# Performance work log

Hardware: AMD Instinct MI355X
Metric: run time of the kernel (lower is better)

Reference implementation:

```python
import jax, jax.numpy as jnp
import numpy as np

N = 8192      # num nodes
E = 131072    # num edges (avg degree 16)
B = 2         # batch
F_NODE = 128
F_EDGE = 64
H = 256       # hidden_dim
L = 3         # num_layers


def setup_inputs() -> dict:
    key = jax.random.key(0)
    ks = jax.random.split(key, 16)
    # unique edges, sorted row-major to match the original i-then-j loop order
    rng = np.random.default_rng(0)
    lin = np.sort(rng.choice(N * N, size=E, replace=False))
    src = jnp.asarray(lin // N, dtype=jnp.int32)
    dst = jnp.asarray(lin % N, dtype=jnp.int32)
    adjacency = jnp.zeros((N, N), jnp.float32).at[src, dst].set(1.0)

    s = 0.05
    return {
        "node_features": jax.random.normal(ks[0], (B, N, F_NODE), jnp.float32),
        "edge_features": jax.random.normal(ks[1], (B, E, F_EDGE), jnp.float32),
        "adjacency": adjacency,
        "src_idx": src,
        "dst_idx": dst,
        "W_ne": jax.random.normal(ks[2], (F_NODE, H), jnp.float32) * s,
        "b_ne": jnp.zeros((H,), jnp.float32),
        "W_ee": jax.random.normal(ks[3], (F_EDGE, H), jnp.float32) * s,
        "b_ee": jnp.zeros((H,), jnp.float32),
        "W_conv": jax.random.normal(ks[4], (L, H, H), jnp.float32) * s,
        "b_conv": jnp.zeros((L, H), jnp.float32),
        "W_cls": jax.random.normal(ks[5], (H, 5), jnp.float32) * s,
        "b_cls": jnp.zeros((5,), jnp.float32),
        "W_ep": jax.random.normal(ks[6], (2 * H, 1), jnp.float32) * s,
        "b_ep": jnp.zeros((1,), jnp.float32),
        "W_gp": jax.random.normal(ks[7], (H, 1), jnp.float32) * s,
        "b_gp": jnp.zeros((1,), jnp.float32),
    }


def reference(node_features, edge_features, adjacency, src_idx, dst_idx,
              W_ne, b_ne, W_ee, b_ee, W_conv, b_conv,
              W_cls, b_cls, W_ep, b_ep, W_gp, b_gp):
    # embeddings (eval mode: dropout is identity)
    h = jax.nn.relu(node_features @ W_ne + b_ne)          # [B,N,H]
    e = jax.nn.relu(edge_features @ W_ee + b_ee)          # [B,E,H] (computed, unused downstream as in original)
    # message-passing layers: messages = A @ h, then linear+relu+residual
    for l in range(L):
        m = jnp.einsum('ij,bjh->bih', adjacency, h)       # dense adjacency matmul
        o = jax.nn.relu(m @ W_conv[l] + b_conv[l])
        h = o + h                                          # residual (in==out dim)
    node_health = h @ W_cls + b_cls                        # [B,N,5]
    # fused edge prediction over all nonzero adjacency entries (row-major order)
    h_src = h[:, src_idx, :]                               # [B,E,H]
    h_dst = h[:, dst_idx, :]                               # [B,E,H]
    edge_repr = jnp.concatenate([h_src, h_dst], axis=-1)   # [B,E,2H]
    edge_propagation = jax.nn.sigmoid(edge_repr @ W_ep + b_ep)  # [B,E,1]
    global_repr = jnp.mean(h, axis=1)                      # [B,H]
    system_health = jax.nn.sigmoid(global_repr @ W_gp + b_gp)   # [B,1]
    return (node_health, edge_propagation, system_health, h)
```

## Files before the change

kernel.cpp:

```cpp
#include <hip/hip_runtime.h>
#include <hip/hip_bf16.h>

typedef __bf16 bf16_t;
typedef __bf16 bf16x8 __attribute__((ext_vector_type(8)));
typedef float f32x4 __attribute__((ext_vector_type(4)));

#define N_NODES 8192
#define N_EDGES 131072
#define HDIM    256


__device__ inline int rowblk_swz(int x) {
  int xcd = x & 7, q = x >> 3;
  return (xcd >> 2) * 128 + (xcd & 3) * 32 + q;
}

__device__ inline float wred(float v) {
#pragma unroll
  for (int m = 32; m; m >>= 1) v += __shfl_xor(v, m);
  return v;
}

__global__ __launch_bounds__(256) void prep_k(const int* __restrict__ src, int* __restrict__ rp,
                                              const float* __restrict__ Wne,
                                              const float* __restrict__ Wconv,
                                              bf16_t* __restrict__ WneT,
                                              bf16_t* __restrict__ WconvT) {
  int x = blockIdx.x, tid = threadIdx.x;
  if (x < 33) {
    int i = x * 256 + tid;
    if (i < N_NODES) {
      int lo = 0, hi = N_EDGES;
      while (lo < hi) { int mid = (lo + hi) >> 1; if (src[mid] < i) lo = mid + 1; else hi = mid; }
      rp[i] = lo;
    } else if (i == N_NODES) {
      rp[i] = N_EDGES;
    }
  } else {
    int t = (x - 33) * 256 + tid;
    if (t < 32768) {
      int n = t / 128, k = t % 128;
      WneT[t] = (bf16_t)Wne[k * 256 + n];
    } else {
      int u = t - 32768;
      int l = u / 65536, r = u % 65536;
      int n = r / 256, k = r % 256;
      WconvT[l * 65536 + n * 256 + k] = (bf16_t)Wconv[l * 65536 + k * 256 + n];
    }
  }
}

__global__ __launch_bounds__(256) void gemm1_k(const float* __restrict__ A,
                                               const bf16_t* __restrict__ BT,
                                               const float* __restrict__ bias,
                                               float* __restrict__ Hout,
                                               bf16_t* __restrict__ S16) {
  int tid = threadIdx.x;
  int lane = tid & 63, wv = tid >> 6;
  int r0 = (rowblk_swz(blockIdx.x) * 4 + wv) * 16;
  int cg0 = blockIdx.y * 64;
  int l15 = lane & 15, l4 = lane >> 4;
  bf16x8 a[4];
  const float* Ap = A + (size_t)(r0 + l15) * 128 + 8 * l4;
#pragma unroll
  for (int kk = 0; kk < 4; ++kk) {
    f32x4 a0 = *(const f32x4*)(Ap + 32 * kk);
    f32x4 a1 = *(const f32x4*)(Ap + 32 * kk + 4);
#pragma unroll
    for (int j = 0; j < 4; ++j) { a[kk][j] = (bf16_t)a0[j]; a[kk][4 + j] = (bf16_t)a1[j]; }
  }
#pragma unroll
  for (int ct = 0; ct < 4; ++ct) {
    int c0 = cg0 + ct * 16;
    const bf16_t* Bp = BT + (size_t)(c0 + l15) * 128 + 8 * l4;
    f32x4 acc = {0.f, 0.f, 0.f, 0.f};
#pragma unroll
    for (int kk = 0; kk < 4; ++kk)
      acc = __builtin_amdgcn_mfma_f32_16x16x32_bf16(a[kk], *(const bf16x8*)(Bp + 32 * kk), acc, 0, 0, 0);
    int col = c0 + l15;
    float bv = bias[col];
#pragma unroll
    for (int i = 0; i < 4; ++i) {
      int row = r0 + 4 * l4 + i;
      size_t idx = (size_t)row * HDIM + col;
      float v = fmaxf(acc[i] + bv, 0.f);
      Hout[idx] = v;
      S16[idx] = (bf16_t)v;
    }
  }
}

__global__ __launch_bounds__(256) void gconv_k(const bf16_t* __restrict__ hs_in,
                                               const int* __restrict__ rp,
                                               const int* __restrict__ dst,
                                               const bf16_t* __restrict__ BT,
                                               const float* __restrict__ bias,
                                               float* __restrict__ Hio,
                                               bf16_t* __restrict__ hs_out) {
  __shared__ bf16_t A_lds[16 * 256];
  int tid = threadIdx.x;
  int x = blockIdx.x;
  int xcd = x & 7, q = x >> 3;
  int b = xcd >> 2;
  int blk = (xcd & 3) * 128 + q;
  int i0 = blk * 16;
  int gang = tid >> 5, l32 = tid & 31;
  const bf16_t* hb = hs_in + (size_t)b * (N_NODES * HDIM) + l32 * 8;
#pragma unroll
  for (int r2 = 0; r2 < 2; ++r2) {
    int lrow = gang * 2 + r2;
    int i = i0 + lrow;
    int e0 = rp[i], e1 = rp[i + 1];
    float acc[8] = {0.f, 0.f, 0.f, 0.f, 0.f, 0.f, 0.f, 0.f};
    int e = e0;
    for (; e + 8 <= e1; e += 8) {
      bf16x8 v[8];
#pragma unroll
      for (int u = 0; u < 8; ++u) v[u] = *(const bf16x8*)(hb + (size_t)dst[e + u] * HDIM);
#pragma unroll
      for (int u = 0; u < 8; ++u)
#pragma unroll
        for (int jj = 0; jj < 8; ++jj) acc[jj] += (float)v[u][jj];
    }
    for (; e < e1; ++e) {
      bf16x8 v = *(const bf16x8*)(hb + (size_t)dst[e] * HDIM);
#pragma unroll
      for (int jj = 0; jj < 8; ++jj) acc[jj] += (float)v[jj];
    }
    bf16x8 o;
#pragma unroll
    for (int jj = 0; jj < 8; ++jj) o[jj] = (bf16_t)acc[jj];
    *(bf16x8*)&A_lds[lrow * 256 + ((l32 ^ (lrow & 7)) * 8)] = o;
  }
  __syncthreads();
  int lane = tid & 63, wv = tid >> 6;
  int l15 = lane & 15, l4 = lane >> 4;
  bf16x8 a[8];
#pragma unroll
  for (int kk = 0; kk < 8; ++kk)
    a[kk] = *(const bf16x8*)&A_lds[l15 * 256 + (((kk * 4 + l4) ^ (l15 & 7)) * 8)];
  int row_base = b * N_NODES + i0;
#pragma unroll
  for (int ct = 0; ct < 4; ++ct) {
    int c0 = wv * 64 + ct * 16;
    const bf16_t* Bp = BT + (size_t)(c0 + l15) * HDIM + 8 * l4;
    f32x4 acc = {0.f, 0.f, 0.f, 0.f};
#pragma unroll
    for (int kk = 0; kk < 8; ++kk)
      acc = __builtin_amdgcn_mfma_f32_16x16x32_bf16(a[kk], *(const bf16x8*)(Bp + 32 * kk), acc, 0, 0, 0);
    int col = c0 + l15;
    float bv = bias[col];
#pragma unroll
    for (int ii = 0; ii < 4; ++ii) {
      int row = row_base + 4 * l4 + ii;
      size_t idx = (size_t)row * HDIM + col;
      float v = fmaxf(acc[ii] + bv, 0.f) + Hio[idx];
      Hio[idx] = v;
      hs_out[idx] = (bf16_t)v;
    }
  }
}

__global__ __launch_bounds__(256) void gconv_heads_k(const bf16_t* __restrict__ hs_in,
                                                     const int* __restrict__ rp,
                                                     const int* __restrict__ dst,
                                                     const bf16_t* __restrict__ BT,
                                                     const float* __restrict__ bias,
                                                     const float* __restrict__ Hio,
                                                     float* __restrict__ out_h,
                                                     const float* __restrict__ Wcls,
                                                     const float* __restrict__ bcls,
                                                     const float* __restrict__ Wep,
                                                     const float* __restrict__ Wgp,
                                                     float* __restrict__ ds,
                                                     float* __restrict__ dd,
                                                     float* __restrict__ pg,
                                                     float* __restrict__ out_nh) {
  __shared__ bf16_t A_lds[16 * 256];
  __shared__ float red[4][16][8];
  __shared__ float pgrow[16];
  int tid = threadIdx.x;
  int x = blockIdx.x;
  int xcd = x & 7, q = x >> 3;
  int b = xcd >> 2;
  int blk = (xcd & 3) * 128 + q;
  int i0 = blk * 16;
  int gang = tid >> 5, l32 = tid & 31;
  const bf16_t* hb = hs_in + (size_t)b * (N_NODES * HDIM) + l32 * 8;
#pragma unroll
  for (int r2 = 0; r2 < 2; ++r2) {
    int lrow = gang * 2 + r2;
    int i = i0 + lrow;
    int e0 = rp[i], e1 = rp[i + 1];
    float acc[8] = {0.f, 0.f, 0.f, 0.f, 0.f, 0.f, 0.f, 0.f};
    int e = e0;
    for (; e + 8 <= e1; e += 8) {
      bf16x8 v[8];
#pragma unroll
      for (int u = 0; u < 8; ++u) v[u] = *(const bf16x8*)(hb + (size_t)dst[e + u] * HDIM);
#pragma unroll
      for (int u = 0; u < 8; ++u)
#pragma unroll
        for (int jj = 0; jj < 8; ++jj) acc[jj] += (float)v[u][jj];
    }
    for (; e < e1; ++e) {
      bf16x8 v = *(const bf16x8*)(hb + (size_t)dst[e] * HDIM);
#pragma unroll
      for (int jj = 0; jj < 8; ++jj) acc[jj] += (float)v[jj];
    }
    bf16x8 o;
#pragma unroll
    for (int jj = 0; jj < 8; ++jj) o[jj] = (bf16_t)acc[jj];
    *(bf16x8*)&A_lds[lrow * 256 + ((l32 ^ (lrow & 7)) * 8)] = o;
  }
  __syncthreads();
  int lane = tid & 63, wv = tid >> 6;
  int l15 = lane & 15, l4 = lane >> 4;
  bf16x8 a[8];
#pragma unroll
  for (int kk = 0; kk < 8; ++kk)
    a[kk] = *(const bf16x8*)&A_lds[l15 * 256 + (((kk * 4 + l4) ^ (l15 & 7)) * 8)];
  int row_base = b * N_NODES + i0;
  float p[4][8];
#pragma unroll
  for (int ii = 0; ii < 4; ++ii)
#pragma unroll
    for (int hh = 0; hh < 8; ++hh) p[ii][hh] = 0.f;
#pragma unroll
  for (int ct = 0; ct < 4; ++ct) {
    int c0 = wv * 64 + ct * 16;
    const bf16_t* Bp = BT + (size_t)(c0 + l15) * HDIM + 8 * l4;
    f32x4 acc = {0.f, 0.f, 0.f, 0.f};
#pragma unroll
    for (int kk = 0; kk < 8; ++kk)
      acc = __builtin_amdgcn_mfma_f32_16x16x32_bf16(a[kk], *(const bf16x8*)(Bp + 32 * kk), acc, 0, 0, 0);
    int col = c0 + l15;
    float bv = bias[col];
    float wc0 = Wcls[col * 5 + 0], wc1 = Wcls[col * 5 + 1], wc2 = Wcls[col * 5 + 2];
    float wc3 = Wcls[col * 5 + 3], wc4 = Wcls[col * 5 + 4];
    float wes = Wep[col], wed = Wep[256 + col], wgv = Wgp[col];
#pragma unroll
    for (int ii = 0; ii < 4; ++ii) {
      int row = row_base + 4 * l4 + ii;
      size_t idx = (size_t)row * HDIM + col;
      float v = fmaxf(acc[ii] + bv, 0.f) + Hio[idx];
      out_h[idx] = v;
      p[ii][0] += v * wc0; p[ii][1] += v * wc1; p[ii][2] += v * wc2;
      p[ii][3] += v * wc3; p[ii][4] += v * wc4;
      p[ii][5] += v * wes; p[ii][6] += v * wed; p[ii][7] += v * wgv;
    }
  }
#pragma unroll
  for (int ii = 0; ii < 4; ++ii)
#pragma unroll
    for (int hh = 0; hh < 8; ++hh) {
      float v = p[ii][hh];
#pragma unroll
      for (int m = 8; m; m >>= 1) v += __shfl_xor(v, m);
      p[ii][hh] = v;
    }
  if (l15 == 0) {
#pragma unroll
    for (int ii = 0; ii < 4; ++ii)
#pragma unroll
      for (int hh = 0; hh < 8; ++hh) red[wv][4 * l4 + ii][hh] = p[ii][hh];
  }
  __syncthreads();
  if (tid < 128) {
    int rl = tid >> 3, hh = tid & 7;
    float s = red[0][rl][hh] + red[1][rl][hh] + red[2][rl][hh] + red[3][rl][hh];
    int grow = row_base + rl;
    if (hh < 5)      out_nh[(size_t)grow * 5 + hh] = s + bcls[hh];
    else if (hh == 5) ds[grow] = s;
    else if (hh == 6) dd[grow] = s;
    else              pgrow[rl] = s;
  }
  __syncthreads();
  if (tid == 0) {
    float t = 0.f;
#pragma unroll
    for (int rl = 0; rl < 16; ++rl) t += pgrow[rl];
    pg[b * 512 + blk] = t;
  }
}

__global__ __launch_bounds__(256) void edge_sys_k(const float* __restrict__ ds,
                                                  const float* __restrict__ dd,
                                                  const int* __restrict__ src,
                                                  const int* __restrict__ dst,
                                                  const float* __restrict__ bep,
                                                  const float* __restrict__ pg,
                                                  const float* __restrict__ bgp,
                                                  float* __restrict__ out_ep,
                                                  float* __restrict__ out_sys) {
  int x = blockIdx.x;
  if (x < 1024) {
    int t = x * 256 + threadIdx.x;
    int b = t >> 17;
    int e = t & (N_EDGES - 1);
    float v = ds[(b << 13) + src[e]] + dd[(b << 13) + dst[e]] + bep[0];
    out_ep[t] = 1.f / (1.f + expf(-v));
  } else {
    int b = x - 1024, t = threadIdx.x;
    float v = pg[b * 512 + t] + pg[b * 512 + 256 + t];
    v = wred(v);
    __shared__ float sm[4];
    if ((t & 63) == 0) sm[t >> 6] = v;
    __syncthreads();
    if (t == 0) {
      float tot = sm[0] + sm[1] + sm[2] + sm[3];
      float g = tot / (float)N_NODES + bgp[0];
      out_sys[b] = 1.f / (1.f + expf(-g));
    }
  }
}

extern "C" void kernel_launch(void* const* d_in, const int* in_sizes, int n_in,
                              void* d_out, int out_size, void* d_ws, size_t ws_size,
                              hipStream_t stream) {
  (void)in_sizes; (void)n_in; (void)out_size; (void)ws_size;
  const float* nf    = (const float*)d_in[0];
  const int*   src   = (const int*)d_in[3];
  const int*   dst   = (const int*)d_in[4];
  const float* Wne   = (const float*)d_in[5];
  const float* bne   = (const float*)d_in[6];
  const float* Wconv = (const float*)d_in[9];
  const float* bconv = (const float*)d_in[10];
  const float* Wcls  = (const float*)d_in[11];
  const float* bcls  = (const float*)d_in[12];
  const float* Wep   = (const float*)d_in[13];
  const float* bep   = (const float*)d_in[14];
  const float* Wgp   = (const float*)d_in[15];
  const float* bgp   = (const float*)d_in[16];

  char* ws = (char*)d_ws;
  float*  h_f32  = (float*)(ws + 0);
  bf16_t* hs0    = (bf16_t*)(ws + 16777216);
  bf16_t* hs1    = (bf16_t*)(ws + 25165824);
  bf16_t* WneT   = (bf16_t*)(ws + 33554432);
  bf16_t* WconvT = (bf16_t*)(ws + 33554432 + 65536);
  int*    rp     = (int*)(ws + 33554432 + 458752);
  float*  ds     = (float*)(ws + 33554432 + 524288);
  float*  dd     = (float*)(ws + 33554432 + 589824);
  float*  pg     = (float*)(ws + 33554432 + 655360);

  float* out     = (float*)d_out;
  float* out_nh  = out;
  float* out_ep  = out + 81920;
  float* out_sys = out + 344064;
  float* out_h   = out + 344066;

  hipLaunchKernelGGL(prep_k, dim3(929), dim3(256), 0, stream, src, rp, Wne, Wconv, WneT, WconvT);
  hipLaunchKernelGGL(gemm1_k, dim3(256, 4), dim3(256), 0, stream, nf, WneT, bne, h_f32, hs0);
  hipLaunchKernelGGL(gconv_k, dim3(1024), dim3(256), 0, stream,
                     hs0, rp, dst, WconvT, bconv, h_f32, hs1);
  hipLaunchKernelGGL(gconv_k, dim3(1024), dim3(256), 0, stream,
                     hs1, rp, dst, WconvT + 65536, bconv + 256, h_f32, hs0);
  hipLaunchKernelGGL(gconv_heads_k, dim3(1024), dim3(256), 0, stream,
                     hs0, rp, dst, WconvT + 131072, bconv + 512, h_f32, out_h,
                     Wcls, bcls, Wep, Wgp, ds, dd, pg, out_nh);
  hipLaunchKernelGGL(edge_sys_k, dim3(1026), dim3(256), 0, stream, ds, dd, src, dst, bep,
                     pg, bgp, out_ep, out_sys);
}
```

Baseline: 127.5 us.

## Fuse prep into first GEMM and drop fp32 hidden-state residual buffer

Merges the prep kernel (row-pointer binary search, Wconv transpose) into the first embedding GEMM launch. Each GEMM block now transposes its Wne slice into swizzled LDS itself, so the separate WneT buffer goes away. The fp32 hidden-state buffer is removed: residuals are read back from the bf16 activations, which cuts fp32 read/write traffic in every conv layer and saves one launch. The cost is lower residual precision, since rounding to bf16 now accumulates across layers, and a small redundant Wne transpose per block.

New measurement: 131.5 us. 3.1% more time.

```diff
diff --git a/kernel.cpp b/kernel.cpp
--- a/kernel.cpp
+++ b/kernel.cpp
@@ -21,47 +21,46 @@
   return v;
 }
 
-__global__ __launch_bounds__(256) void prep_k(const int* __restrict__ src, int* __restrict__ rp,
-                                              const float* __restrict__ Wne,
-                                              const float* __restrict__ Wconv,
-                                              bf16_t* __restrict__ WneT,
-                                              bf16_t* __restrict__ WconvT) {
+__global__ __launch_bounds__(256) void gemm1_prep_k(const float* __restrict__ nf,
+                                                    const float* __restrict__ Wne,
+                                                    const float* __restrict__ bne,
+                                                    const float* __restrict__ Wconv,
+                                                    const int* __restrict__ src,
+                                                    int* __restrict__ rp,
+                                                    bf16_t* __restrict__ WconvT,
+                                                    bf16_t* __restrict__ hs0) {
   int x = blockIdx.x, tid = threadIdx.x;
-  if (x < 33) {
-    int i = x * 256 + tid;
-    if (i < N_NODES) {
-      int lo = 0, hi = N_EDGES;
-      while (lo < hi) { int mid = (lo + hi) >> 1; if (src[mid] < i) lo = mid + 1; else hi = mid; }
-      rp[i] = lo;
-    } else if (i == N_NODES) {
-      rp[i] = N_EDGES;
-    }
-  } else {
-    int t = (x - 33) * 256 + tid;
-    if (t < 32768) {
-      int n = t / 128, k = t % 128;
-      WneT[t] = (bf16_t)Wne[k * 256 + n];
+  if (x >= 1024) {
+    if (x < 1057) {
+      int i = (x - 1024) * 256 + tid;
+      if (i < N_NODES) {
+        int lo = 0, hi = N_EDGES;
+        while (lo < hi) { int mid = (lo + hi) >> 1; if (src[mid] < i) lo = mid + 1; else hi = mid; }
+        rp[i] = lo;
+      } else if (i == N_NODES) {
+        rp[i] = N_EDGES;
+      }
     } else {
-      int u = t - 32768;
+      int u = (x - 1057) * 256 + tid;
       int l = u / 65536, r = u % 65536;
       int n = r / 256, k = r % 256;
       WconvT[l * 65536 + n * 256 + k] = (bf16_t)Wconv[l * 65536 + k * 256 + n];
     }
-  }
-}
-
-__global__ __launch_bounds__(256) void gemm1_k(const float* __restrict__ A,
-                                               const bf16_t* __restrict__ BT,
-                                               const float* __restrict__ bias,
-                                               float* __restrict__ Hout,
-                                               bf16_t* __restrict__ S16) {
-  int tid = threadIdx.x;
+    return;
+  }
+  __shared__ bf16_t Wlds[64 * 128];
+  int xb = x & 255, yb = x >> 8;
+  int cg0 = yb * 64;
+  for (int k = tid >> 6; k < 128; k += 4) {
+    int lc = tid & 63;
+    float w = Wne[k * 256 + cg0 + lc];
+    Wlds[lc * 128 + (((k >> 3) ^ (lc & 15)) << 3) + (k & 7)] = (bf16_t)w;
+  }
   int lane = tid & 63, wv = tid >> 6;
-  int r0 = (rowblk_swz(blockIdx.x) * 4 + wv) * 16;
-  int cg0 = blockIdx.y * 64;
+  int r0 = (rowblk_swz(xb) * 4 + wv) * 16;
   int l15 = lane & 15, l4 = lane >> 4;
   bf16x8 a[4];
-  const float* Ap = A + (size_t)(r0 + l15) * 128 + 8 * l4;
+  const float* Ap = nf + (size_t)(r0 + l15) * 128 + 8 * l4;
 #pragma unroll
   for (int kk = 0; kk < 4; ++kk) {
     f32x4 a0 = *(const f32x4*)(Ap + 32 * kk);
@@ -69,23 +68,23 @@
 #pragma unroll
     for (int j = 0; j < 4; ++j) { a[kk][j] = (bf16_t)a0[j]; a[kk][4 + j] = (bf16_t)a1[j]; }
   }
+  __syncthreads();
 #pragma unroll
   for (int ct = 0; ct < 4; ++ct) {
-    int c0 = cg0 + ct * 16;
-    const bf16_t* Bp = BT + (size_t)(c0 + l15) * 128 + 8 * l4;
+    int lc0 = ct * 16;
     f32x4 acc = {0.f, 0.f, 0.f, 0.f};
 #pragma unroll
-    for (int kk = 0; kk < 4; ++kk)
-      acc = __builtin_amdgcn_mfma_f32_16x16x32_bf16(a[kk], *(const bf16x8*)(Bp + 32 * kk), acc, 0, 0, 0);
-    int col = c0 + l15;
-    float bv = bias[col];
+    for (int kk = 0; kk < 4; ++kk) {
+      bf16x8 b = *(const bf16x8*)&Wlds[(lc0 + l15) * 128 + (((4 * kk + l4) ^ l15) << 3)];
+      acc = __builtin_amdgcn_mfma_f32_16x16x32_bf16(a[kk], b, acc, 0, 0, 0);
+    }
+    int col = cg0 + lc0 + l15;
+    float bv = bne[col];
 #pragma unroll
     for (int i = 0; i < 4; ++i) {
       int row = r0 + 4 * l4 + i;
       size_t idx = (size_t)row * HDIM + col;
-      float v = fmaxf(acc[i] + bv, 0.f);
-      Hout[idx] = v;
-      S16[idx] = (bf16_t)v;
+      hs0[idx] = (bf16_t)fmaxf(acc[i] + bv, 0.f);
     }
   }
 }
@@ -95,7 +94,6 @@
                                                const int* __restrict__ dst,
                                                const bf16_t* __restrict__ BT,
                                                const float* __restrict__ bias,
-                                               float* __restrict__ Hio,
                                                bf16_t* __restrict__ hs_out) {
   __shared__ bf16_t A_lds[16 * 256];
   int tid = threadIdx.x;
@@ -154,8 +152,7 @@
     for (int ii = 0; ii < 4; ++ii) {
       int row = row_base + 4 * l4 + ii;
       size_t idx = (size_t)row * HDIM + col;
-      float v = fmaxf(acc[ii] + bv, 0.f) + Hio[idx];
-      Hio[idx] = v;
+      float v = fmaxf(acc[ii] + bv, 0.f) + (float)hs_in[idx];
       hs_out[idx] = (bf16_t)v;
     }
   }
@@ -166,7 +163,6 @@
                                                      const int* __restrict__ dst,
                                                      const bf16_t* __restrict__ BT,
                                                      const float* __restrict__ bias,
-                                                     const float* __restrict__ Hio,
                                                      float* __restrict__ out_h,
                                                      const float* __restrict__ Wcls,
                                                      const float* __restrict__ bcls,
@@ -243,7 +239,7 @@
     for (int ii = 0; ii < 4; ++ii) {
       int row = row_base + 4 * l4 + ii;
       size_t idx = (size_t)row * HDIM + col;
-      float v = fmaxf(acc[ii] + bv, 0.f) + Hio[idx];
+      float v = fmaxf(acc[ii] + bv, 0.f) + (float)hs_in[idx];
       out_h[idx] = v;
       p[ii][0] += v * wc0; p[ii][1] += v * wc1; p[ii][2] += v * wc2;
       p[ii][3] += v * wc3; p[ii][4] += v * wc4;
@@ -334,15 +330,13 @@
   const float* bgp   = (const float*)d_in[16];
 
   char* ws = (char*)d_ws;
-  float*  h_f32  = (float*)(ws + 0);
-  bf16_t* hs0    = (bf16_t*)(ws + 16777216);
-  bf16_t* hs1    = (bf16_t*)(ws + 25165824);
-  bf16_t* WneT   = (bf16_t*)(ws + 33554432);
-  bf16_t* WconvT = (bf16_t*)(ws + 33554432 + 65536);
-  int*    rp     = (int*)(ws + 33554432 + 458752);
-  float*  ds     = (float*)(ws + 33554432 + 524288);
-  float*  dd     = (float*)(ws + 33554432 + 589824);
-  float*  pg     = (float*)(ws + 33554432 + 655360);
+  bf16_t* hs0    = (bf16_t*)(ws + 0);
+  bf16_t* hs1    = (bf16_t*)(ws + 8388608);
+  bf16_t* WconvT = (bf16_t*)(ws + 16777216);
+  int*    rp     = (int*)(ws + 17170432);
+  float*  ds     = (float*)(ws + 17207296);
+  float*  dd     = (float*)(ws + 17272832);
+  float*  pg     = (float*)(ws + 17338368);
 
   float* out     = (float*)d_out;
   float* out_nh  = out;
@@ -350,14 +344,14 @@
   float* out_sys = out + 344064;
   float* out_h   = out + 344066;
 
-  hipLaunchKernelGGL(prep_k, dim3(929), dim3(256), 0, stream, src, rp, Wne, Wconv, WneT, WconvT);
-  hipLaunchKernelGGL(gemm1_k, dim3(256, 4), dim3(256), 0, stream, nf, WneT, bne, h_f32, hs0);
+  hipLaunchKernelGGL(gemm1_prep_k, dim3(1825), dim3(256), 0, stream,
+                     nf, Wne, bne, Wconv, src, rp, WconvT, hs0);
   hipLaunchKernelGGL(gconv_k, dim3(1024), dim3(256), 0, stream,
-                     hs0, rp, dst, WconvT, bconv, h_f32, hs1);
+                     hs0, rp, dst, WconvT, bconv, hs1);
   hipLaunchKernelGGL(gconv_k, dim3(1024), dim3(256), 0, stream,
-                     hs1, rp, dst, WconvT + 65536, bconv + 256, h_f32, hs0);
+                     hs1, rp, dst, WconvT + 65536, bconv + 256, hs0);
   hipLaunchKernelGGL(gconv_heads_k, dim3(1024), dim3(256), 0, stream,
-                     hs0, rp, dst, WconvT + 131072, bconv + 512, h_f32, out_h,
+                     hs0, rp, dst, WconvT + 131072, bconv + 512, out_h,
                      Wcls, bcls, Wep, Wgp, ds, dd, pg, out_nh);
   hipLaunchKernelGGL(edge_sys_k, dim3(1026), dim3(256), 0, stream, ds, dd, src, dst, bep,
                      pg, bgp, out_ep, out_sys);
```
